# Performance work log

Measured on AMD Instinct MI355X. Metric: run time of the kernel, lower is better.

## Reference

```python
import jax, jax.numpy as jnp
import numpy as np

DIM = 1024
HEADS = 16
DIM_HEAD = 64
INNER = HEADS * DIM_HEAD  # 1024
SCALE = DIM_HEAD ** (-0.5)
EPS = 1e-5


def _layernorm(x, g, b):
    mu = jnp.mean(x, axis=-1, keepdims=True)
    var = jnp.mean(jnp.square(x - mu), axis=-1, keepdims=True)
    return (x - mu) * jax.lax.rsqrt(var + EPS) * g + b


def _split_heads(t):
    # b t n (h d) -> b h t n d
    b, T, n, _ = t.shape
    return t.reshape(b, T, n, HEADS, DIM_HEAD).transpose(0, 3, 1, 2, 4)


def setup_inputs() -> dict:
    key = jax.random.key(0)
    ks = jax.random.split(key, 9)
    b, T, n1, n2 = 8, 4, 1024, 64
    x = jax.random.normal(ks[0], (b, T, n1, DIM), dtype=jnp.float32)
    latents = jax.random.normal(ks[1], (b, T, n2, DIM), dtype=jnp.float32)
    g_media = 1.0 + 0.02 * jax.random.normal(ks[2], (DIM,), dtype=jnp.float32)
    b_media = 0.02 * jax.random.normal(ks[3], (DIM,), dtype=jnp.float32)
    g_lat = 1.0 + 0.02 * jax.random.normal(ks[4], (DIM,), dtype=jnp.float32)
    b_lat = 0.02 * jax.random.normal(ks[5], (DIM,), dtype=jnp.float32)
    s = DIM ** (-0.5)
    Wq = jax.random.normal(ks[6], (DIM, INNER), dtype=jnp.float32) * s
    Wkv = jax.random.normal(ks[7], (DIM, 2 * INNER), dtype=jnp.float32) * s
    Wo = jax.random.normal(ks[8], (INNER, DIM), dtype=jnp.float32) * (INNER ** (-0.5))
    return {"x": x, "latents": latents, "g_media": g_media, "b_media": b_media,
            "g_lat": g_lat, "b_lat": b_lat, "Wq": Wq, "Wkv": Wkv, "Wo": Wo}


def reference(x, latents, g_media, b_media, g_lat, b_lat, Wq, Wkv, Wo):
    x = _layernorm(x, g_media, b_media)          # (b, T, n1, D)
    lat = _layernorm(latents, g_lat, b_lat)      # (b, T, n2, D)

    q = lat @ Wq                                 # (b, T, n2, inner)
    kv_input = jnp.concatenate((x, lat), axis=-2)  # (b, T, n1+n2, D)
    kv = kv_input @ Wkv                          # (b, T, n1+n2, 2*inner)
    k, v = jnp.split(kv, 2, axis=-1)

    q = _split_heads(q) * SCALE                  # (b, h, T, n2, d)
    k = _split_heads(k)                          # (b, h, T, n1+n2, d)
    v = _split_heads(v)

    sim = jnp.einsum('bhtid,bhtjd->bhtij', q, k)  # (b, h, T, n2, n1+n2)
    attn = jax.nn.softmax(sim, axis=-1)           # stable (amax subtracted)
    out = jnp.einsum('bhtij,bhtjd->bhtid', attn, v)

    # b h t n d -> b t n (h d)
    b, h, T, n, d = out.shape
    out = out.transpose(0, 2, 3, 1, 4).reshape(b, T, n, h * d)
    return out @ Wo
```

## Files before the change

kernel.cpp:

```cpp
#include <hip/hip_runtime.h>

#define DEVI __device__ __forceinline__

typedef unsigned short u16;
typedef unsigned int u32;

using bf16x8 = __attribute__((ext_vector_type(8))) short;
using f32x4  = __attribute__((ext_vector_type(4))) float;

DEVI u16 f2bf(float f) {
  u32 u = __builtin_bit_cast(u32, f);
  u32 r = (u + 0x7fffu + ((u >> 16) & 1u)) >> 16;
  return (u16)r;
}

DEVI void gl_lds16(const u16* g, u16* l) {
  __builtin_amdgcn_global_load_lds(
      (const __attribute__((address_space(1))) u32*)g,
      (__attribute__((address_space(3))) u32*)l, 16, 0, 0);
}

__global__ __launch_bounds__(256) void ln_kernel(
    const float* __restrict__ x, const float* __restrict__ lat,
    const float* __restrict__ gm, const float* __restrict__ bm,
    const float* __restrict__ gl, const float* __restrict__ bl,
    u16* __restrict__ kvin, u16* __restrict__ latb)
{
  int row = blockIdx.x;
  int bt = row / 1088, r = row % 1088;
  const float *src, *g, *b;
  bool is_lat = (r >= 1024);
  if (!is_lat) { src = x + ((size_t)bt*1024 + r)*1024; g = gm; b = bm; }
  else         { src = lat + ((size_t)bt*64 + (r-1024))*1024; g = gl; b = bl; }
  int tid = threadIdx.x;
  float4 v = *(const float4*)(src + tid*4);
  float s1 = v.x+v.y+v.z+v.w;
  float s2 = v.x*v.x+v.y*v.y+v.z*v.z+v.w*v.w;
  for (int off=32; off; off>>=1){ s1 += __shfl_down(s1,off); s2 += __shfl_down(s2,off); }
  __shared__ float red[2][4];
  int w = tid>>6, lane = tid&63;
  if (lane==0){ red[0][w]=s1; red[1][w]=s2; }
  __syncthreads();
  s1 = red[0][0]+red[0][1]+red[0][2]+red[0][3];
  s2 = red[1][0]+red[1][1]+red[1][2]+red[1][3];
  float mu = s1 * (1.f/1024.f);
  float var = s2 * (1.f/1024.f) - mu*mu;
  float rstd = rsqrtf(var + 1e-5f);
  float4 gv = *(const float4*)(g + tid*4);
  float4 bv = *(const float4*)(b + tid*4);
  ushort4 o;
  o.x = f2bf((v.x-mu)*rstd*gv.x + bv.x);
  o.y = f2bf((v.y-mu)*rstd*gv.y + bv.y);
  o.z = f2bf((v.z-mu)*rstd*gv.z + bv.z);
  o.w = f2bf((v.w-mu)*rstd*gv.w + bv.w);
  *(ushort4*)(kvin + (size_t)row*1024 + tid*4) = o;
  if (is_lat) *(ushort4*)(latb + ((size_t)(bt*64 + (r-1024)))*1024 + tid*4) = o;
}

__global__ __launch_bounds__(256) void transpose_all(
    const float* __restrict__ Wq, const float* __restrict__ Wkv,
    const float* __restrict__ Wo,
    u16* __restrict__ wqT, u16* __restrict__ wkvT, u16* __restrict__ woT)
{
  __shared__ float t[32][33];
  int bxg = blockIdx.x;
  const float* in; u16* outp; int C, bxi;
  if (bxg < 32)      { in = Wq;  outp = wqT;  C = 1024; bxi = bxg; }
  else if (bxg < 96) { in = Wkv; outp = wkvT; C = 2048; bxi = bxg - 32; }
  else               { in = Wo;  outp = woT;  C = 1024; bxi = bxg - 96; }
  const int R = 1024;
  int bx = bxi*32, by = blockIdx.y*32;
  int tx = threadIdx.x & 31, ty = threadIdx.x >> 5;
  for (int k=0;k<32;k+=8) t[ty+k][tx] = in[(size_t)(by+ty+k)*C + bx+tx];
  __syncthreads();
  for (int k=0;k<32;k+=8) outp[(size_t)(bx+ty+k)*R + by+tx] = f2bf(t[tx][ty+k]);
}

__global__ __launch_bounds__(512,2) void gemm256_kvq(
    const u16* __restrict__ A, const u16* __restrict__ BT,
    const u16* __restrict__ Aq, const u16* __restrict__ BTq,
    u16* __restrict__ kb, u16* __restrict__ vt, u16* __restrict__ qb)
{
  __shared__ u16 lds[2][2][2][256][32];
  const int tid = threadIdx.x;
  const int w = tid>>6, lane = tid&63;
  const int li = lane&15, lg = lane>>4;
  const int wm = w>>2, wn = w&3;
  const int bid = blockIdx.x;
  const int swz = (bid&7)*140 + (bid>>3);
  const bool is_q = (swz >= 1088);
  const u16* Asrc; const u16* Bsrc; int m0, n0;
  if (!is_q) { Asrc = A;  Bsrc = BT;  m0 = (swz>>3)*256;        n0 = (swz&7)*256; }
  else       { int qt = swz-1088; Asrc = Aq; Bsrc = BTq; m0 = (qt>>2)*256; n0 = (qt&3)*256; }
  const int srow = lane>>2;
  const int scol = ((lane&3) ^ ((lane>>3)&3))*8;
  const int rchunk = (lg ^ ((li>>1)&3))*8;

#define STAGE(b, mat, kh, kt) do {                                            \
    const u16* _s = (mat) ? Bsrc : Asrc;                                      \
    const int _base = (mat) ? n0 : m0;                                        \
    _Pragma("unroll")                                                         \
    for (int L=0; L<2; ++L) {                                                 \
      const int _r = L*128 + w*16;                                            \
      gl_lds16(_s + (size_t)(_base + _r + srow)*1024 + (kt)*64 + (kh)*32 + scol, \
               &lds[b][mat][kh][_r][0]);                                      \
    }                                                                         \
  } while(0)
#define BARRIER() asm volatile("s_barrier" ::: "memory")
#define LGKM0()   do { asm volatile("s_waitcnt lgkmcnt(0)" ::: "memory"); \
                       __builtin_amdgcn_sched_barrier(0); } while(0)
#define VM4()     asm volatile("s_waitcnt vmcnt(4)" ::: "memory")

  f32x4 acc[8][4] = {};

  STAGE(0,0,0,0); STAGE(0,1,0,0); STAGE(0,0,1,0); STAGE(0,1,1,0);
  VM4(); BARRIER();

  for (int j=0; j<16; ++j) {
    const int c = j&1;
    const int kt = (j<15) ? j+1 : 15;
    bf16x8 a[4], b0[4], b1[4];

    #pragma unroll
    for (int mf=0; mf<4; ++mf)
      a[mf] = *(const bf16x8*)&lds[c][0][0][wm*128 + mf*16 + li][rchunk];
    #pragma unroll
    for (int nf=0; nf<4; ++nf)
      b0[nf] = *(const bf16x8*)&lds[c][1][0][wn*64 + nf*16 + li][rchunk];
    STAGE(c^1,0,0,kt);
    BARRIER(); LGKM0();
    __builtin_amdgcn_s_setprio(1);
    #pragma unroll
    for (int mf=0; mf<4; ++mf)
      #pragma unroll
      for (int nf=0; nf<4; ++nf)
        acc[mf][nf] = __builtin_amdgcn_mfma_f32_16x16x32_bf16(a[mf], b0[nf], acc[mf][nf], 0,0,0);
    __builtin_amdgcn_s_setprio(0);
    BARRIER();

    #pragma unroll
    for (int mf=0; mf<4; ++mf)
      a[mf] = *(const bf16x8*)&lds[c][0][0][wm*128 + 64 + mf*16 + li][rchunk];
    STAGE(c^1,1,0,kt);
    VM4();
    BARRIER(); LGKM0();
    __builtin_amdgcn_s_setprio(1);
    #pragma unroll
    for (int mf=0; mf<4; ++mf)
      #pragma unroll
      for (int nf=0; nf<4; ++nf)
        acc[4+mf][nf] = __builtin_amdgcn_mfma_f32_16x16x32_bf16(a[mf], b0[nf], acc[4+mf][nf], 0,0,0);
    __builtin_amdgcn_s_setprio(0);
    BARRIER();

    #pragma unroll
    for (int mf=0; mf<4; ++mf)
      a[mf] = *(const bf16x8*)&lds[c][0][1][wm*128 + mf*16 + li][rchunk];
    #pragma unroll
    for (int nf=0; nf<4; ++nf)
      b1[nf] = *(const bf16x8*)&lds[c][1][1][wn*64 + nf*16 + li][rchunk];
    STAGE(c^1,0,1,kt);
    BARRIER(); LGKM0();
    __builtin_amdgcn_s_setprio(1);
    #pragma unroll
    for (int mf=0; mf<4; ++mf)
      #pragma unroll
      for (int nf=0; nf<4; ++nf)
        acc[mf][nf] = __builtin_amdgcn_mfma_f32_16x16x32_bf16(a[mf], b1[nf], acc[mf][nf], 0,0,0);
    __builtin_amdgcn_s_setprio(0);
    BARRIER();

    #pragma unroll
    for (int mf=0; mf<4; ++mf)
      a[mf] = *(const bf16x8*)&lds[c][0][1][wm*128 + 64 + mf*16 + li][rchunk];
    STAGE(c^1,1,1,kt);
    VM4();
    BARRIER(); LGKM0();
    __builtin_amdgcn_s_setprio(1);
    #pragma unroll
    for (int mf=0; mf<4; ++mf)
      #pragma unroll
      for (int nf=0; nf<4; ++nf)
        acc[4+mf][nf] = __builtin_amdgcn_mfma_f32_16x16x32_bf16(a[mf], b1[nf], acc[4+mf][nf], 0,0,0);
    __builtin_amdgcn_s_setprio(0);
    BARRIER();
  }
#undef STAGE
#undef BARRIER
#undef LGKM0
#undef VM4

  if (is_q) {
    #pragma unroll
    for (int am=0; am<8; ++am)
      #pragma unroll
      for (int nf=0; nf<4; ++nf) {
        int row = m0 + wm*128 + am*16 + lg*4;
        int col = n0 + wn*64 + nf*16 + li;
        #pragma unroll
        for (int rg=0; rg<4; ++rg)
          qb[(size_t)(row+rg)*1024 + col] = f2bf(acc[am][nf][rg]*0.125f);
      }
  } else if (n0 < 1024) {
    #pragma unroll
    for (int am=0; am<8; ++am)
      #pragma unroll
      for (int nf=0; nf<4; ++nf) {
        int row = m0 + wm*128 + am*16 + lg*4;
        int col = n0 + wn*64 + nf*16 + li;
        #pragma unroll
        for (int rg=0; rg<4; ++rg)
          kb[(size_t)(row+rg)*1024 + col] = f2bf(acc[am][nf][rg]);
      }
  } else {
    #pragma unroll
    for (int am=0; am<8; ++am)
      #pragma unroll
      for (int nf=0; nf<4; ++nf) {
        int r0 = m0 + wm*128 + am*16 + lg*4;
        int cc = n0 + wn*64 + nf*16 + li - 1024;
        int bt = r0/1088, jj = r0 - bt*1088;
        ushort4 o;
        o.x = f2bf(acc[am][nf][0]); o.y = f2bf(acc[am][nf][1]);
        o.z = f2bf(acc[am][nf][2]); o.w = f2bf(acc[am][nf][3]);
        *(ushort4*)(vt + ((size_t)(bt*1024 + cc))*1088 + jj) = o;
      }
  }
}

__global__ __launch_bounds__(256,4) void gemm_out(
    const u16* __restrict__ A, const u16* __restrict__ BT,
    float* __restrict__ C)
{
  __shared__ u16 lA[128*32];
  __shared__ u16 lB[64*32];
  const int tid = threadIdx.x;
  const int w = tid>>6, lane = tid&63;
  const int li = lane&15, lg = lane>>4;
  const int wm = w>>1, wn = w&1;
  int m0 = blockIdx.y*128, n0 = blockIdx.x*64;
  const int srow = tid>>2;
  const int scol = ((tid&3) ^ ((tid>>3)&3))*8;
  const int rchunk = (lg ^ ((li>>1)&3))*8;
  u16* dA0 = lA + (w*16)*32;
  u16* dA1 = lA + (64 + w*16)*32;
  u16* dB  = lB + (w*16)*32;
  const u16* pa0 = A  + (size_t)(m0 + srow)*1024 + scol;
  const u16* pa1 = A  + (size_t)(m0 + 64 + srow)*1024 + scol;
  const u16* pb  = BT + (size_t)(n0 + srow)*1024 + scol;
  f32x4 acc[4][2] = {};
  for (int k=0; k<32; ++k) {
    gl_lds16(pa0 + k*32, dA0);
    gl_lds16(pa1 + k*32, dA1);
    if (srow < 64) gl_lds16(pb + k*32, dB);
    __syncthreads();
    bf16x8 af[4], bf[2];
    #pragma unroll
    for (int m=0;m<4;++m) af[m] = *(const bf16x8*)(lA + (wm*64 + m*16 + li)*32 + rchunk);
    #pragma unroll
    for (int n=0;n<2;++n) bf[n] = *(const bf16x8*)(lB + (wn*32 + n*16 + li)*32 + rchunk);
    #pragma unroll
    for (int m=0;m<4;++m)
      #pragma unroll
      for (int n=0;n<2;++n)
        acc[m][n] = __builtin_amdgcn_mfma_f32_16x16x32_bf16(af[m], bf[n], acc[m][n], 0,0,0);
    __syncthreads();
  }
  #pragma unroll
  for (int m=0;m<4;++m)
    #pragma unroll
    for (int n=0;n<2;++n) {
      int row = m0 + wm*64 + m*16 + lg*4;
      int col = n0 + wn*32 + n*16 + li;
      #pragma unroll
      for (int rg=0;rg<4;++rg)
        C[(size_t)(row+rg)*1024 + col] = acc[m][n][rg];
    }
}

__global__ __launch_bounds__(256,2) void attn_kernel(
    const u16* __restrict__ qbuf, const u16* __restrict__ kbuf,
    const u16* __restrict__ vT, u16* __restrict__ aout)
{
  __shared__ u16 kv_lds[2][2][64][64];
  __shared__ u16 p_im[4][16][72];
  int blk = blockIdx.x;
  int bt = blk >> 4, h = blk & 15;
  int w = threadIdx.x>>6, lane = threadIdx.x&63;
  int li = lane&15, lg = lane>>4;
  const u16* qrow = qbuf + ((size_t)(bt*64 + w*16 + li))*1024 + h*64;
  bf16x8 qf0 = *(const bf16x8*)(qrow + lg*8);
  bf16x8 qf1 = *(const bf16x8*)(qrow + 32 + lg*8);
  const int srl = lane>>3;
  const int sch = (lane&7) ^ srl;
  const u16* kgbase = kbuf + ((size_t)(bt*1088) + w*16 + srl)*1024 + h*64 + sch*8;
  const u16* vgbase = vT + ((size_t)(bt*1024 + h*64 + w*16 + srl))*1088 + sch*8;
  const int rc0 = ((lg     ^ (li&7)))*8;
  const int rc1 = (((4+lg) ^ (li&7)))*8;

#define STAGE_KV(b, c) do {                                                    \
    int _j0 = (c)*64;                                                          \
    _Pragma("unroll")                                                          \
    for (int i=0;i<2;++i) {                                                    \
      gl_lds16(kgbase + (size_t)(_j0 + i*8)*1024, &kv_lds[b][0][w*16+i*8][0]); \
      gl_lds16(vgbase + _j0 + (size_t)(i*8)*1088, &kv_lds[b][1][w*16+i*8][0]); \
    }                                                                          \
  } while(0)

  float mrun = -INFINITY, lrun = 0.f;
  f32x4 oacc[4] = {};

  STAGE_KV(0,0);
  __syncthreads();

  for (int c=0; c<17; ++c) {
    int cb = c&1;
    if (c<16) STAGE_KV(cb^1, c+1);
    const u16* kl = &kv_lds[cb][0][0][0];
    const u16* vl = &kv_lds[cb][1][0][0];
    f32x4 s[4] = {};
    #pragma unroll
    for (int jt=0; jt<4; ++jt) {
      const u16* kr = kl + (jt*16+li)*64;
      bf16x8 k0 = *(const bf16x8*)(kr + rc0);
      bf16x8 k1 = *(const bf16x8*)(kr + rc1);
      s[jt] = __builtin_amdgcn_mfma_f32_16x16x32_bf16(k0, qf0, s[jt], 0,0,0);
      s[jt] = __builtin_amdgcn_mfma_f32_16x16x32_bf16(k1, qf1, s[jt], 0,0,0);
    }
    float cm = -INFINITY;
    #pragma unroll
    for (int jt=0;jt<4;++jt)
      cm = fmaxf(cm, fmaxf(fmaxf(s[jt][0], s[jt][1]), fmaxf(s[jt][2], s[jt][3])));
    cm = fmaxf(cm, __shfl_xor(cm,16));
    cm = fmaxf(cm, __shfl_xor(cm,32));
    float mnew = fmaxf(mrun, cm);
    float sf = __expf(mrun - mnew);
    float ls = 0.f;
    #pragma unroll
    for (int jt=0;jt<4;++jt) {
      float p0 = __expf(s[jt][0]-mnew), p1 = __expf(s[jt][1]-mnew);
      float p2 = __expf(s[jt][2]-mnew), p3 = __expf(s[jt][3]-mnew);
      ls += p0+p1+p2+p3;
      ushort4 pk; pk.x = f2bf(p0); pk.y = f2bf(p1); pk.z = f2bf(p2); pk.w = f2bf(p3);
      *(ushort4*)&p_im[w][li][jt*16 + lg*4] = pk;
    }
    ls += __shfl_xor(ls,16);
    ls += __shfl_xor(ls,32);
    lrun = lrun*sf + ls;
    mrun = mnew;
    float sfr[4];
    #pragma unroll
    for (int rg=0;rg<4;++rg) sfr[rg] = __shfl(sf, lg*4+rg);
    #pragma unroll
    for (int dt=0;dt<4;++dt) {
      oacc[dt][0]*=sfr[0]; oacc[dt][1]*=sfr[1]; oacc[dt][2]*=sfr[2]; oacc[dt][3]*=sfr[3];
    }
    bf16x8 pa0 = *(const bf16x8*)&p_im[w][li][lg*8];
    bf16x8 pa1 = *(const bf16x8*)&p_im[w][li][32 + lg*8];
    #pragma unroll
    for (int dt=0;dt<4;++dt) {
      const u16* vr = vl + (dt*16+li)*64;
      bf16x8 v0 = *(const bf16x8*)(vr + rc0);
      bf16x8 v1 = *(const bf16x8*)(vr + rc1);
      oacc[dt] = __builtin_amdgcn_mfma_f32_16x16x32_bf16(pa0, v0, oacc[dt], 0,0,0);
      oacc[dt] = __builtin_amdgcn_mfma_f32_16x16x32_bf16(pa1, v1, oacc[dt], 0,0,0);
    }
    __syncthreads();
  }
#undef STAGE_KV

  float linv[4];
  #pragma unroll
  for (int rg=0;rg<4;++rg) linv[rg] = 1.f / __shfl(lrun, lg*4+rg);
  u16* orow = aout + ((size_t)(bt*64 + w*16))*1024 + h*64;
  #pragma unroll
  for (int dt=0;dt<4;++dt)
    #pragma unroll
    for (int rg=0;rg<4;++rg)
      orow[(size_t)(lg*4+rg)*1024 + dt*16 + li] = f2bf(oacc[dt][rg]*linv[rg]);
}

extern "C" void kernel_launch(void* const* d_in, const int* in_sizes, int n_in,
                              void* d_out, int out_size, void* d_ws, size_t ws_size,
                              hipStream_t stream) {
  const float* x   = (const float*)d_in[0];
  const float* lat = (const float*)d_in[1];
  const float* gm  = (const float*)d_in[2];
  const float* bm  = (const float*)d_in[3];
  const float* gl  = (const float*)d_in[4];
  const float* bl  = (const float*)d_in[5];
  const float* Wq  = (const float*)d_in[6];
  const float* Wkv = (const float*)d_in[7];
  const float* Wo  = (const float*)d_in[8];
  float* out = (float*)d_out;

  char* ws = (char*)d_ws;
  const size_t KV_BYTES = (size_t)32*1088*1024*2;
  u16* kvin = (u16*)(ws);
  u16* kbuf = (u16*)(ws + KV_BYTES);
  u16* vT   = (u16*)(ws + 2*KV_BYTES);
  u16* latb = (u16*)(ws + 3*KV_BYTES);
  u16* qbuf = (u16*)(ws + 3*KV_BYTES + (size_t)4194304);
  u16* aout = (u16*)(ws + 3*KV_BYTES + (size_t)2*4194304);
  u16* wqT  = (u16*)(ws + 3*KV_BYTES + (size_t)3*4194304);
  u16* wkvT = (u16*)(ws + 3*KV_BYTES + (size_t)3*4194304 + 2097152);
  u16* woT  = (u16*)(ws + 3*KV_BYTES + (size_t)3*4194304 + 2097152 + 4194304);

  ln_kernel<<<dim3(32*1088), dim3(256), 0, stream>>>(x, lat, gm, bm, gl, bl, kvin, latb);
  transpose_all<<<dim3(128,32), dim3(256), 0, stream>>>(Wq, Wkv, Wo, wqT, wkvT, woT);

  gemm256_kvq<<<dim3(1120), dim3(512), 0, stream>>>(kvin, wkvT, latb, wqT, kbuf, vT, qbuf);
  attn_kernel<<<dim3(512), dim3(256), 0, stream>>>(qbuf, kbuf, vT, aout);
  gemm_out<<<dim3(16,16), dim3(256), 0, stream>>>(aout, woT, out);
}
```

Baseline: 262.6 us.

## Merge layernorm and weight transpose launches; rebalance KV GEMM grid with half tiles

The weight-transpose work is folded into the layernorm kernel as extra blocks, which removes one launch and lets both jobs run concurrently. The KV/Q GEMM grid changes from 1120 full 256x256 tiles to 1024 full tiles plus 192 half-height (128-row) tiles that cover the last M rows. The aim is to fit the grid to whole waves of CUs and cut the tail imbalance. The cost is branching inside the GEMM loop and more complex tile indexing.

```diff
diff --git a/kernel.cpp b/kernel.cpp
--- a/kernel.cpp
+++ b/kernel.cpp
@@ -20,12 +20,31 @@
       (__attribute__((address_space(3))) u32*)l, 16, 0, 0);
 }
 
-__global__ __launch_bounds__(256) void ln_kernel(
+__global__ __launch_bounds__(256) void ln_tr_kernel(
     const float* __restrict__ x, const float* __restrict__ lat,
     const float* __restrict__ gm, const float* __restrict__ bm,
     const float* __restrict__ gl, const float* __restrict__ bl,
-    u16* __restrict__ kvin, u16* __restrict__ latb)
+    const float* __restrict__ Wq, const float* __restrict__ Wkv,
+    const float* __restrict__ Wo,
+    u16* __restrict__ kvin, u16* __restrict__ latb,
+    u16* __restrict__ wqT, u16* __restrict__ wkvT, u16* __restrict__ woT)
 {
+  __shared__ float tshm[32][33];
+  __shared__ float red[2][4];
+  if (blockIdx.x >= 34816) {
+    int t = blockIdx.x - 34816;
+    int bxg = t & 127, gy = t >> 7;
+    const float* in; u16* outp; int C, bxi;
+    if (bxg < 32)      { in = Wq;  outp = wqT;  C = 1024; bxi = bxg; }
+    else if (bxg < 96) { in = Wkv; outp = wkvT; C = 2048; bxi = bxg - 32; }
+    else               { in = Wo;  outp = woT;  C = 1024; bxi = bxg - 96; }
+    int bx = bxi*32, by = gy*32;
+    int tx = threadIdx.x & 31, ty = threadIdx.x >> 5;
+    for (int k=0;k<32;k+=8) tshm[ty+k][tx] = in[(size_t)(by+ty+k)*C + bx+tx];
+    __syncthreads();
+    for (int k=0;k<32;k+=8) outp[(size_t)(bx+ty+k)*1024 + by+tx] = f2bf(tshm[tx][ty+k]);
+    return;
+  }
   int row = blockIdx.x;
   int bt = row / 1088, r = row % 1088;
   const float *src, *g, *b;
@@ -37,7 +56,6 @@
   float s1 = v.x+v.y+v.z+v.w;
   float s2 = v.x*v.x+v.y*v.y+v.z*v.z+v.w*v.w;
   for (int off=32; off; off>>=1){ s1 += __shfl_down(s1,off); s2 += __shfl_down(s2,off); }
-  __shared__ float red[2][4];
   int w = tid>>6, lane = tid&63;
   if (lane==0){ red[0][w]=s1; red[1][w]=s2; }
   __syncthreads();
@@ -57,25 +75,6 @@
   if (is_lat) *(ushort4*)(latb + ((size_t)(bt*64 + (r-1024)))*1024 + tid*4) = o;
 }
 
-__global__ __launch_bounds__(256) void transpose_all(
-    const float* __restrict__ Wq, const float* __restrict__ Wkv,
-    const float* __restrict__ Wo,
-    u16* __restrict__ wqT, u16* __restrict__ wkvT, u16* __restrict__ woT)
-{
-  __shared__ float t[32][33];
-  int bxg = blockIdx.x;
-  const float* in; u16* outp; int C, bxi;
-  if (bxg < 32)      { in = Wq;  outp = wqT;  C = 1024; bxi = bxg; }
-  else if (bxg < 96) { in = Wkv; outp = wkvT; C = 2048; bxi = bxg - 32; }
-  else               { in = Wo;  outp = woT;  C = 1024; bxi = bxg - 96; }
-  const int R = 1024;
-  int bx = bxi*32, by = blockIdx.y*32;
-  int tx = threadIdx.x & 31, ty = threadIdx.x >> 5;
-  for (int k=0;k<32;k+=8) t[ty+k][tx] = in[(size_t)(by+ty+k)*C + bx+tx];
-  __syncthreads();
-  for (int k=0;k<32;k+=8) outp[(size_t)(bx+ty+k)*R + by+tx] = f2bf(t[tx][ty+k]);
-}
-
 __global__ __launch_bounds__(512,2) void gemm256_kvq(
     const u16* __restrict__ A, const u16* __restrict__ BT,
     const u16* __restrict__ Aq, const u16* __restrict__ BTq,
@@ -87,11 +86,19 @@
   const int li = lane&15, lg = lane>>4;
   const int wm = w>>2, wn = w&3;
   const int bid = blockIdx.x;
-  const int swz = (bid&7)*140 + (bid>>3);
-  const bool is_q = (swz >= 1088);
-  const u16* Asrc; const u16* Bsrc; int m0, n0;
-  if (!is_q) { Asrc = A;  Bsrc = BT;  m0 = (swz>>3)*256;        n0 = (swz&7)*256; }
-  else       { int qt = swz-1088; Asrc = Aq; Bsrc = BTq; m0 = (qt>>2)*256; n0 = (qt&3)*256; }
+  bool half = false, is_q = false;
+  const u16 *Asrc, *Bsrc; int m0, n0;
+  if (bid < 1024) {
+    int swz = (bid&7)*128 + (bid>>3);
+    if (swz < 992) { Asrc = A; Bsrc = BT; m0 = (swz>>3)*256; n0 = (swz&7)*256; }
+    else { is_q = true; int qt = swz-992; Asrc = Aq; Bsrc = BTq; m0 = (qt>>2)*256; n0 = (qt&3)*256; }
+  } else {
+    int t = bid - 1024;
+    int swz = (t&7)*24 + (t>>3);
+    half = true; Asrc = A; Bsrc = BT;
+    m0 = 31744 + (swz>>3)*128; n0 = (swz&7)*256;
+  }
+  const int wrowbase = half ? wm*64 : wm*128;
   const int srow = lane>>2;
   const int scol = ((lane&3) ^ ((lane>>3)&3))*8;
   const int rchunk = (lg ^ ((li>>1)&3))*8;
@@ -123,7 +130,7 @@
 
     #pragma unroll
     for (int mf=0; mf<4; ++mf)
-      a[mf] = *(const bf16x8*)&lds[c][0][0][wm*128 + mf*16 + li][rchunk];
+      a[mf] = *(const bf16x8*)&lds[c][0][0][wrowbase + mf*16 + li][rchunk];
     #pragma unroll
     for (int nf=0; nf<4; ++nf)
       b0[nf] = *(const bf16x8*)&lds[c][1][0][wn*64 + nf*16 + li][rchunk];
@@ -138,24 +145,28 @@
     __builtin_amdgcn_s_setprio(0);
     BARRIER();
 
-    #pragma unroll
-    for (int mf=0; mf<4; ++mf)
-      a[mf] = *(const bf16x8*)&lds[c][0][0][wm*128 + 64 + mf*16 + li][rchunk];
+    if (!half) {
+      #pragma unroll
+      for (int mf=0; mf<4; ++mf)
+        a[mf] = *(const bf16x8*)&lds[c][0][0][wrowbase + 64 + mf*16 + li][rchunk];
+    }
     STAGE(c^1,1,0,kt);
     VM4();
     BARRIER(); LGKM0();
-    __builtin_amdgcn_s_setprio(1);
+    if (!half) {
+      __builtin_amdgcn_s_setprio(1);
+      #pragma unroll
+      for (int mf=0; mf<4; ++mf)
+        #pragma unroll
+        for (int nf=0; nf<4; ++nf)
+          acc[4+mf][nf] = __builtin_amdgcn_mfma_f32_16x16x32_bf16(a[mf], b0[nf], acc[4+mf][nf], 0,0,0);
+      __builtin_amdgcn_s_setprio(0);
+    }
+    BARRIER();
+
     #pragma unroll
     for (int mf=0; mf<4; ++mf)
-      #pragma unroll
-      for (int nf=0; nf<4; ++nf)
-        acc[4+mf][nf] = __builtin_amdgcn_mfma_f32_16x16x32_bf16(a[mf], b0[nf], acc[4+mf][nf], 0,0,0);
-    __builtin_amdgcn_s_setprio(0);
-    BARRIER();
-
-    #pragma unroll
-    for (int mf=0; mf<4; ++mf)
-      a[mf] = *(const bf16x8*)&lds[c][0][1][wm*128 + mf*16 + li][rchunk];
+      a[mf] = *(const bf16x8*)&lds[c][0][1][wrowbase + mf*16 + li][rchunk];
     #pragma unroll
     for (int nf=0; nf<4; ++nf)
       b1[nf] = *(const bf16x8*)&lds[c][1][1][wn*64 + nf*16 + li][rchunk];
@@ -170,19 +181,23 @@
     __builtin_amdgcn_s_setprio(0);
     BARRIER();
 
-    #pragma unroll
-    for (int mf=0; mf<4; ++mf)
-      a[mf] = *(const bf16x8*)&lds[c][0][1][wm*128 + 64 + mf*16 + li][rchunk];
+    if (!half) {
+      #pragma unroll
+      for (int mf=0; mf<4; ++mf)
+        a[mf] = *(const bf16x8*)&lds[c][0][1][wrowbase + 64 + mf*16 + li][rchunk];
+    }
     STAGE(c^1,1,1,kt);
     VM4();
     BARRIER(); LGKM0();
-    __builtin_amdgcn_s_setprio(1);
-    #pragma unroll
-    for (int mf=0; mf<4; ++mf)
-      #pragma unroll
-      for (int nf=0; nf<4; ++nf)
-        acc[4+mf][nf] = __builtin_amdgcn_mfma_f32_16x16x32_bf16(a[mf], b1[nf], acc[4+mf][nf], 0,0,0);
-    __builtin_amdgcn_s_setprio(0);
+    if (!half) {
+      __builtin_amdgcn_s_setprio(1);
+      #pragma unroll
+      for (int mf=0; mf<4; ++mf)
+        #pragma unroll
+        for (int nf=0; nf<4; ++nf)
+          acc[4+mf][nf] = __builtin_amdgcn_mfma_f32_16x16x32_bf16(a[mf], b1[nf], acc[4+mf][nf], 0,0,0);
+      __builtin_amdgcn_s_setprio(0);
+    }
     BARRIER();
   }
 #undef STAGE
@@ -190,6 +205,7 @@
 #undef LGKM0
 #undef VM4
 
+  const int amN = half ? 4 : 8;
   if (is_q) {
     #pragma unroll
     for (int am=0; am<8; ++am)
@@ -202,22 +218,20 @@
           qb[(size_t)(row+rg)*1024 + col] = f2bf(acc[am][nf][rg]*0.125f);
       }
   } else if (n0 < 1024) {
-    #pragma unroll
-    for (int am=0; am<8; ++am)
+    for (int am=0; am<amN; ++am)
       #pragma unroll
       for (int nf=0; nf<4; ++nf) {
-        int row = m0 + wm*128 + am*16 + lg*4;
+        int row = m0 + wrowbase + am*16 + lg*4;
         int col = n0 + wn*64 + nf*16 + li;
         #pragma unroll
         for (int rg=0; rg<4; ++rg)
           kb[(size_t)(row+rg)*1024 + col] = f2bf(acc[am][nf][rg]);
       }
   } else {
-    #pragma unroll
-    for (int am=0; am<8; ++am)
+    for (int am=0; am<amN; ++am)
       #pragma unroll
       for (int nf=0; nf<4; ++nf) {
-        int r0 = m0 + wm*128 + am*16 + lg*4;
+        int r0 = m0 + wrowbase + am*16 + lg*4;
         int cc = n0 + wn*64 + nf*16 + li - 1024;
         int bt = r0/1088, jj = r0 - bt*1088;
         ushort4 o;
@@ -406,10 +420,10 @@
   u16* wkvT = (u16*)(ws + 3*KV_BYTES + (size_t)3*4194304 + 2097152);
   u16* woT  = (u16*)(ws + 3*KV_BYTES + (size_t)3*4194304 + 2097152 + 4194304);
 
-  ln_kernel<<<dim3(32*1088), dim3(256), 0, stream>>>(x, lat, gm, bm, gl, bl, kvin, latb);
-  transpose_all<<<dim3(128,32), dim3(256), 0, stream>>>(Wq, Wkv, Wo, wqT, wkvT, woT);
-
-  gemm256_kvq<<<dim3(1120), dim3(512), 0, stream>>>(kvin, wkvT, latb, wqT, kbuf, vT, qbuf);
+  ln_tr_kernel<<<dim3(38912), dim3(256), 0, stream>>>(
+      x, lat, gm, bm, gl, bl, Wq, Wkv, Wo, kvin, latb, wqT, wkvT, woT);
+
+  gemm256_kvq<<<dim3(1216), dim3(512), 0, stream>>>(kvin, wkvT, latb, wqT, kbuf, vT, qbuf);
   attn_kernel<<<dim3(512), dim3(256), 0, stream>>>(qbuf, kbuf, vT, aout);
   gemm_out<<<dim3(16,16), dim3(256), 0, stream>>>(aout, woT, out);
 }
```

Measured after the change: 991.3 us. 3.77x slower.

## Make KV/Q GEMM persistent with cross-tile prefetch; merge layernorm and weight transpose launches

Applied to the files above, without the earlier changes.

The KV/Q projection GEMM becomes a persistent kernel with 256 blocks, each looping over 4–5 of the 1120 tiles. The last k-step of each tile prefetches the first k-slice of the next tile, so the pipeline does not drain between tiles. The layernorm and weight-transpose kernels are merged into one launch to save a kernel launch and its tail. The cost is that the epilogue stores now sit inside the loop and serialize with the next tile's compute. The 256-block grid is also unbalanced (96 blocks do 5 tiles, the rest 4), which may leave CUs idle at the end.

```diff
diff --git a/kernel.cpp b/kernel.cpp
--- a/kernel.cpp
+++ b/kernel.cpp
@@ -20,12 +20,31 @@
       (__attribute__((address_space(3))) u32*)l, 16, 0, 0);
 }
 
-__global__ __launch_bounds__(256) void ln_kernel(
+__global__ __launch_bounds__(256) void ln_tr_kernel(
     const float* __restrict__ x, const float* __restrict__ lat,
     const float* __restrict__ gm, const float* __restrict__ bm,
     const float* __restrict__ gl, const float* __restrict__ bl,
-    u16* __restrict__ kvin, u16* __restrict__ latb)
+    const float* __restrict__ Wq, const float* __restrict__ Wkv,
+    const float* __restrict__ Wo,
+    u16* __restrict__ kvin, u16* __restrict__ latb,
+    u16* __restrict__ wqT, u16* __restrict__ wkvT, u16* __restrict__ woT)
 {
+  __shared__ float tshm[32][33];
+  __shared__ float red[2][4];
+  if (blockIdx.x >= 34816) {
+    int t = blockIdx.x - 34816;
+    int bxg = t & 127, gy = t >> 7;
+    const float* in; u16* outp; int C, bxi;
+    if (bxg < 32)      { in = Wq;  outp = wqT;  C = 1024; bxi = bxg; }
+    else if (bxg < 96) { in = Wkv; outp = wkvT; C = 2048; bxi = bxg - 32; }
+    else               { in = Wo;  outp = woT;  C = 1024; bxi = bxg - 96; }
+    int bx = bxi*32, by = gy*32;
+    int tx = threadIdx.x & 31, ty = threadIdx.x >> 5;
+    for (int k=0;k<32;k+=8) tshm[ty+k][tx] = in[(size_t)(by+ty+k)*C + bx+tx];
+    __syncthreads();
+    for (int k=0;k<32;k+=8) outp[(size_t)(bx+ty+k)*1024 + by+tx] = f2bf(tshm[tx][ty+k]);
+    return;
+  }
   int row = blockIdx.x;
   int bt = row / 1088, r = row % 1088;
   const float *src, *g, *b;
@@ -37,7 +56,6 @@
   float s1 = v.x+v.y+v.z+v.w;
   float s2 = v.x*v.x+v.y*v.y+v.z*v.z+v.w*v.w;
   for (int off=32; off; off>>=1){ s1 += __shfl_down(s1,off); s2 += __shfl_down(s2,off); }
-  __shared__ float red[2][4];
   int w = tid>>6, lane = tid&63;
   if (lane==0){ red[0][w]=s1; red[1][w]=s2; }
   __syncthreads();
@@ -57,25 +75,6 @@
   if (is_lat) *(ushort4*)(latb + ((size_t)(bt*64 + (r-1024)))*1024 + tid*4) = o;
 }
 
-__global__ __launch_bounds__(256) void transpose_all(
-    const float* __restrict__ Wq, const float* __restrict__ Wkv,
-    const float* __restrict__ Wo,
-    u16* __restrict__ wqT, u16* __restrict__ wkvT, u16* __restrict__ woT)
-{
-  __shared__ float t[32][33];
-  int bxg = blockIdx.x;
-  const float* in; u16* outp; int C, bxi;
-  if (bxg < 32)      { in = Wq;  outp = wqT;  C = 1024; bxi = bxg; }
-  else if (bxg < 96) { in = Wkv; outp = wkvT; C = 2048; bxi = bxg - 32; }
-  else               { in = Wo;  outp = woT;  C = 1024; bxi = bxg - 96; }
-  const int R = 1024;
-  int bx = bxi*32, by = blockIdx.y*32;
-  int tx = threadIdx.x & 31, ty = threadIdx.x >> 5;
-  for (int k=0;k<32;k+=8) t[ty+k][tx] = in[(size_t)(by+ty+k)*C + bx+tx];
-  __syncthreads();
-  for (int k=0;k<32;k+=8) outp[(size_t)(bx+ty+k)*R + by+tx] = f2bf(t[tx][ty+k]);
-}
-
 __global__ __launch_bounds__(512,2) void gemm256_kvq(
     const u16* __restrict__ A, const u16* __restrict__ BT,
     const u16* __restrict__ Aq, const u16* __restrict__ BTq,
@@ -87,18 +86,19 @@
   const int li = lane&15, lg = lane>>4;
   const int wm = w>>2, wn = w&3;
   const int bid = blockIdx.x;
-  const int swz = (bid&7)*140 + (bid>>3);
-  const bool is_q = (swz >= 1088);
-  const u16* Asrc; const u16* Bsrc; int m0, n0;
-  if (!is_q) { Asrc = A;  Bsrc = BT;  m0 = (swz>>3)*256;        n0 = (swz&7)*256; }
-  else       { int qt = swz-1088; Asrc = Aq; Bsrc = BTq; m0 = (qt>>2)*256; n0 = (qt&3)*256; }
+  const int nt = (bid < 96) ? 5 : 4;
   const int srow = lane>>2;
   const int scol = ((lane&3) ^ ((lane>>3)&3))*8;
   const int rchunk = (lg ^ ((li>>1)&3))*8;
 
-#define STAGE(b, mat, kh, kt) do {                                            \
-    const u16* _s = (mat) ? Bsrc : Asrc;                                      \
-    const int _base = (mat) ? n0 : m0;                                        \
+#define RESOLVE(t, As, Bs, M0, N0, ISQ) do {                                  \
+    int _swz = ((t)&7)*140 + ((t)>>3);                                        \
+    if (_swz < 1088) { ISQ=false; As=A; Bs=BT; M0=(_swz>>3)*256; N0=(_swz&7)*256; } \
+    else { ISQ=true; int _qt=_swz-1088; As=Aq; Bs=BTq; M0=(_qt>>2)*256; N0=(_qt&3)*256; } \
+  } while(0)
+#define STAGE(b, mat, kh, kt, SA, SB, M0_, N0_) do {                          \
+    const u16* _s = (mat) ? (SB) : (SA);                                      \
+    const int _base = (mat) ? (N0_) : (M0_);                                  \
     _Pragma("unroll")                                                         \
     for (int L=0; L<2; ++L) {                                                 \
       const int _r = L*128 + w*16;                                            \
@@ -111,121 +111,137 @@
                        __builtin_amdgcn_sched_barrier(0); } while(0)
 #define VM4()     asm volatile("s_waitcnt vmcnt(4)" ::: "memory")
 
-  f32x4 acc[8][4] = {};
-
-  STAGE(0,0,0,0); STAGE(0,1,0,0); STAGE(0,0,1,0); STAGE(0,1,1,0);
+  const u16 *Asrc, *Bsrc, *AsrcN, *BsrcN;
+  int m0, n0, m0N, n0N; bool is_q, is_qN;
+  RESOLVE(bid, Asrc, Bsrc, m0, n0, is_q);
+
+  STAGE(0,0,0,0, Asrc,Bsrc,m0,n0); STAGE(0,1,0,0, Asrc,Bsrc,m0,n0);
+  STAGE(0,0,1,0, Asrc,Bsrc,m0,n0); STAGE(0,1,1,0, Asrc,Bsrc,m0,n0);
   VM4(); BARRIER();
 
-  for (int j=0; j<16; ++j) {
-    const int c = j&1;
-    const int kt = (j<15) ? j+1 : 15;
-    bf16x8 a[4], b0[4], b1[4];
-
-    #pragma unroll
-    for (int mf=0; mf<4; ++mf)
-      a[mf] = *(const bf16x8*)&lds[c][0][0][wm*128 + mf*16 + li][rchunk];
-    #pragma unroll
-    for (int nf=0; nf<4; ++nf)
-      b0[nf] = *(const bf16x8*)&lds[c][1][0][wn*64 + nf*16 + li][rchunk];
-    STAGE(c^1,0,0,kt);
-    BARRIER(); LGKM0();
-    __builtin_amdgcn_s_setprio(1);
-    #pragma unroll
-    for (int mf=0; mf<4; ++mf)
+  for (int tk=0; tk<nt; ++tk) {
+    const int tnext = (tk+1<nt) ? bid+(tk+1)*256 : bid+tk*256;
+    RESOLVE(tnext, AsrcN, BsrcN, m0N, n0N, is_qN);
+
+    f32x4 acc[8][4] = {};
+    for (int j=0; j<16; ++j) {
+      const int c = j&1;
+      const u16* sA = (j<15) ? Asrc : AsrcN;
+      const u16* sB = (j<15) ? Bsrc : BsrcN;
+      const int bM = (j<15) ? m0 : m0N;
+      const int bN = (j<15) ? n0 : n0N;
+      const int kt = (j<15) ? j+1 : 0;
+      bf16x8 a[4], b0[4], b1[4];
+
+      #pragma unroll
+      for (int mf=0; mf<4; ++mf)
+        a[mf] = *(const bf16x8*)&lds[c][0][0][wm*128 + mf*16 + li][rchunk];
       #pragma unroll
       for (int nf=0; nf<4; ++nf)
-        acc[mf][nf] = __builtin_amdgcn_mfma_f32_16x16x32_bf16(a[mf], b0[nf], acc[mf][nf], 0,0,0);
-    __builtin_amdgcn_s_setprio(0);
-    BARRIER();
-
-    #pragma unroll
-    for (int mf=0; mf<4; ++mf)
-      a[mf] = *(const bf16x8*)&lds[c][0][0][wm*128 + 64 + mf*16 + li][rchunk];
-    STAGE(c^1,1,0,kt);
-    VM4();
-    BARRIER(); LGKM0();
-    __builtin_amdgcn_s_setprio(1);
-    #pragma unroll
-    for (int mf=0; mf<4; ++mf)
+        b0[nf] = *(const bf16x8*)&lds[c][1][0][wn*64 + nf*16 + li][rchunk];
+      STAGE(c^1,0,0,kt, sA,sB,bM,bN);
+      BARRIER(); LGKM0();
+      __builtin_amdgcn_s_setprio(1);
+      #pragma unroll
+      for (int mf=0; mf<4; ++mf)
+        #pragma unroll
+        for (int nf=0; nf<4; ++nf)
+          acc[mf][nf] = __builtin_amdgcn_mfma_f32_16x16x32_bf16(a[mf], b0[nf], acc[mf][nf], 0,0,0);
+      __builtin_amdgcn_s_setprio(0);
+      BARRIER();
+
+      #pragma unroll
+      for (int mf=0; mf<4; ++mf)
+        a[mf] = *(const bf16x8*)&lds[c][0][0][wm*128 + 64 + mf*16 + li][rchunk];
+      STAGE(c^1,1,0,kt, sA,sB,bM,bN);
+      VM4();
+      BARRIER(); LGKM0();
+      __builtin_amdgcn_s_setprio(1);
+      #pragma unroll
+      for (int mf=0; mf<4; ++mf)
+        #pragma unroll
+        for (int nf=0; nf<4; ++nf)
+          acc[4+mf][nf] = __builtin_amdgcn_mfma_f32_16x16x32_bf16(a[mf], b0[nf], acc[4+mf][nf], 0,0,0);
+      __builtin_amdgcn_s_setprio(0);
+      BARRIER();
+
+      #pragma unroll
+      for (int mf=0; mf<4; ++mf)
+        a[mf] = *(const bf16x8*)&lds[c][0][1][wm*128 + mf*16 + li][rchunk];
       #pragma unroll
       for (int nf=0; nf<4; ++nf)
-        acc[4+mf][nf] = __builtin_amdgcn_mfma_f32_16x16x32_bf16(a[mf], b0[nf], acc[4+mf][nf], 0,0,0);
-    __builtin_amdgcn_s_setprio(0);
-    BARRIER();
-
-    #pragma unroll
-    for (int mf=0; mf<4; ++mf)
-      a[mf] = *(const bf16x8*)&lds[c][0][1][wm*128 + mf*16 + li][rchunk];
-    #pragma unroll
-    for (int nf=0; nf<4; ++nf)
-      b1[nf] = *(const bf16x8*)&lds[c][1][1][wn*64 + nf*16 + li][rchunk];
-    STAGE(c^1,0,1,kt);
-    BARRIER(); LGKM0();
-    __builtin_amdgcn_s_setprio(1);
-    #pragma unroll
-    for (int mf=0; mf<4; ++mf)
-      #pragma unroll
-      for (int nf=0; nf<4; ++nf)
-        acc[mf][nf] = __builtin_amdgcn_mfma_f32_16x16x32_bf16(a[mf], b1[nf], acc[mf][nf], 0,0,0);
-    __builtin_amdgcn_s_setprio(0);
-    BARRIER();
-
-    #pragma unroll
-    for (int mf=0; mf<4; ++mf)
-      a[mf] = *(const bf16x8*)&lds[c][0][1][wm*128 + 64 + mf*16 + li][rchunk];
-    STAGE(c^1,1,1,kt);
-    VM4();
-    BARRIER(); LGKM0();
-    __builtin_amdgcn_s_setprio(1);
-    #pragma unroll
-    for (int mf=0; mf<4; ++mf)
-      #pragma unroll
-      for (int nf=0; nf<4; ++nf)
-        acc[4+mf][nf] = __builtin_amdgcn_mfma_f32_16x16x32_bf16(a[mf], b1[nf], acc[4+mf][nf], 0,0,0);
-    __builtin_amdgcn_s_setprio(0);
-    BARRIER();
+        b1[nf] = *(const bf16x8*)&lds[c][1][1][wn*64 + nf*16 + li][rchunk];
+      STAGE(c^1,0,1,kt, sA,sB,bM,bN);
+      BARRIER(); LGKM0();
+      __builtin_amdgcn_s_setprio(1);
+      #pragma unroll
+      for (int mf=0; mf<4; ++mf)
+        #pragma unroll
+        for (int nf=0; nf<4; ++nf)
+          acc[mf][nf] = __builtin_amdgcn_mfma_f32_16x16x32_bf16(a[mf], b1[nf], acc[mf][nf], 0,0,0);
+      __builtin_amdgcn_s_setprio(0);
+      BARRIER();
+
+      #pragma unroll
+      for (int mf=0; mf<4; ++mf)
+        a[mf] = *(const bf16x8*)&lds[c][0][1][wm*128 + 64 + mf*16 + li][rchunk];
+      STAGE(c^1,1,1,kt, sA,sB,bM,bN);
+      VM4();
+      BARRIER(); LGKM0();
+      __builtin_amdgcn_s_setprio(1);
+      #pragma unroll
+      for (int mf=0; mf<4; ++mf)
+        #pragma unroll
+        for (int nf=0; nf<4; ++nf)
+          acc[4+mf][nf] = __builtin_amdgcn_mfma_f32_16x16x32_bf16(a[mf], b1[nf], acc[4+mf][nf], 0,0,0);
+      __builtin_amdgcn_s_setprio(0);
+      BARRIER();
+    }
+
+    if (is_q) {
+      #pragma unroll
+      for (int am=0; am<8; ++am)
+        #pragma unroll
+        for (int nf=0; nf<4; ++nf) {
+          int row = m0 + wm*128 + am*16 + lg*4;
+          int col = n0 + wn*64 + nf*16 + li;
+          #pragma unroll
+          for (int rg=0; rg<4; ++rg)
+            qb[(size_t)(row+rg)*1024 + col] = f2bf(acc[am][nf][rg]*0.125f);
+        }
+    } else if (n0 < 1024) {
+      #pragma unroll
+      for (int am=0; am<8; ++am)
+        #pragma unroll
+        for (int nf=0; nf<4; ++nf) {
+          int row = m0 + wm*128 + am*16 + lg*4;
+          int col = n0 + wn*64 + nf*16 + li;
+          #pragma unroll
+          for (int rg=0; rg<4; ++rg)
+            kb[(size_t)(row+rg)*1024 + col] = f2bf(acc[am][nf][rg]);
+        }
+    } else {
+      #pragma unroll
+      for (int am=0; am<8; ++am)
+        #pragma unroll
+        for (int nf=0; nf<4; ++nf) {
+          int r0 = m0 + wm*128 + am*16 + lg*4;
+          int cc = n0 + wn*64 + nf*16 + li - 1024;
+          int bt = r0/1088, jj = r0 - bt*1088;
+          ushort4 o;
+          o.x = f2bf(acc[am][nf][0]); o.y = f2bf(acc[am][nf][1]);
+          o.z = f2bf(acc[am][nf][2]); o.w = f2bf(acc[am][nf][3]);
+          *(ushort4*)(vt + ((size_t)(bt*1024 + cc))*1088 + jj) = o;
+        }
+    }
+
+    Asrc = AsrcN; Bsrc = BsrcN; m0 = m0N; n0 = n0N; is_q = is_qN;
   }
+#undef RESOLVE
 #undef STAGE
 #undef BARRIER
 #undef LGKM0
 #undef VM4
-
-  if (is_q) {
-    #pragma unroll
-    for (int am=0; am<8; ++am)
-      #pragma unroll
-      for (int nf=0; nf<4; ++nf) {
-        int row = m0 + wm*128 + am*16 + lg*4;
-        int col = n0 + wn*64 + nf*16 + li;
-        #pragma unroll
-        for (int rg=0; rg<4; ++rg)
-          qb[(size_t)(row+rg)*1024 + col] = f2bf(acc[am][nf][rg]*0.125f);
-      }
-  } else if (n0 < 1024) {
-    #pragma unroll
-    for (int am=0; am<8; ++am)
-      #pragma unroll
-      for (int nf=0; nf<4; ++nf) {
-        int row = m0 + wm*128 + am*16 + lg*4;
-        int col = n0 + wn*64 + nf*16 + li;
-        #pragma unroll
-        for (int rg=0; rg<4; ++rg)
-          kb[(size_t)(row+rg)*1024 + col] = f2bf(acc[am][nf][rg]);
-      }
-  } else {
-    #pragma unroll
-    for (int am=0; am<8; ++am)
-      #pragma unroll
-      for (int nf=0; nf<4; ++nf) {
-        int r0 = m0 + wm*128 + am*16 + lg*4;
-        int cc = n0 + wn*64 + nf*16 + li - 1024;
-        int bt = r0/1088, jj = r0 - bt*1088;
-        ushort4 o;
-        o.x = f2bf(acc[am][nf][0]); o.y = f2bf(acc[am][nf][1]);
-        o.z = f2bf(acc[am][nf][2]); o.w = f2bf(acc[am][nf][3]);
-        *(ushort4*)(vt + ((size_t)(bt*1024 + cc))*1088 + jj) = o;
-      }
-  }
 }
 
 __global__ __launch_bounds__(256,4) void gemm_out(
@@ -406,10 +422,10 @@
   u16* wkvT = (u16*)(ws + 3*KV_BYTES + (size_t)3*4194304 + 2097152);
   u16* woT  = (u16*)(ws + 3*KV_BYTES + (size_t)3*4194304 + 2097152 + 4194304);
 
-  ln_kernel<<<dim3(32*1088), dim3(256), 0, stream>>>(x, lat, gm, bm, gl, bl, kvin, latb);
-  transpose_all<<<dim3(128,32), dim3(256), 0, stream>>>(Wq, Wkv, Wo, wqT, wkvT, woT);
-
-  gemm256_kvq<<<dim3(1120), dim3(512), 0, stream>>>(kvin, wkvT, latb, wqT, kbuf, vT, qbuf);
+  ln_tr_kernel<<<dim3(38912), dim3(256), 0, stream>>>(
+      x, lat, gm, bm, gl, bl, Wq, Wkv, Wo, kvin, latb, wqT, wkvT, woT);
+
+  gemm256_kvq<<<dim3(256), dim3(512), 0, stream>>>(kvin, wkvT, latb, wqT, kbuf, vT, qbuf);
   attn_kernel<<<dim3(512), dim3(256), 0, stream>>>(qbuf, kbuf, vT, aout);
   gemm_out<<<dim3(16,16), dim3(256), 0, stream>>>(aout, woT, out);
 }
```

New measurement: 266.8 us. Within noise of the previous version (+1.6%).
